# Optimization experiments

Hardware: AMD Instinct MI355X
Metric: run time of the kernel (lower is better)

Reference implementation:

```python
import jax, jax.numpy as jnp
import numpy as np

S, B, DM, H, DFF = 2048, 4, 1024, 16, 4096
DK = DM // H  # 64, dv == dk
EPS = 1e-5

def layer_norm(x, g, b):
    mu = jnp.mean(x, axis=-1, keepdims=True)
    var = jnp.var(x, axis=-1, keepdims=True)
    return (x - mu) * jax.lax.rsqrt(var + EPS) * g + b

def setup_inputs() -> dict:
    key = jax.random.key(0)
    ks = jax.random.split(key, 12)
    sc = 0.02
    return {
        "X": jax.random.normal(ks[0], (S, B, DM), dtype=jnp.float32),
        # stacked per-head projections: weight [H, dk, dm], bias [H, dk]
        "WQ_w": jax.random.normal(ks[1], (H, DK, DM), dtype=jnp.float32) * sc,
        "WQ_b": jnp.zeros((H, DK), dtype=jnp.float32),
        "WK_w": jax.random.normal(ks[2], (H, DK, DM), dtype=jnp.float32) * sc,
        "WK_b": jnp.zeros((H, DK), dtype=jnp.float32),
        "WV_w": jax.random.normal(ks[3], (H, DK, DM), dtype=jnp.float32) * sc,
        "WV_b": jnp.zeros((H, DK), dtype=jnp.float32),
        "WO_w": jax.random.normal(ks[4], (DM, H * DK), dtype=jnp.float32) * sc,
        "WO_b": jnp.zeros((DM,), dtype=jnp.float32),
        "ln1_g": jnp.ones((DM,), dtype=jnp.float32),
        "ln1_b": jnp.zeros((DM,), dtype=jnp.float32),
        "W1": jax.random.normal(ks[5], (DFF, DM), dtype=jnp.float32) * sc,
        "b1": jnp.zeros((DFF,), dtype=jnp.float32),
        "W2": jax.random.normal(ks[6], (DM, DFF), dtype=jnp.float32) * sc,
        "b2": jnp.zeros((DM,), dtype=jnp.float32),
        "ln2_g": jnp.ones((DM,), dtype=jnp.float32),
        "ln2_b": jnp.zeros((DM,), dtype=jnp.float32),
    }

def reference(X, WQ_w, WQ_b, WK_w, WK_b, WV_w, WV_b, WO_w, WO_b,
              ln1_g, ln1_b, W1, b1, W2, b2, ln2_g, ln2_b):
    # --- self-attention (encoder: no causal mask, no key_mask, drop=0) ---
    # X: [S, B, DM]; per-head Q/K/V: [S, B, H, DK]
    Q = jnp.einsum('sbd,hkd->sbhk', X, WQ_w) + WQ_b
    K = jnp.einsum('sbd,hkd->sbhk', X, WK_w) + WK_b
    V = jnp.einsum('sbd,hvd->sbhv', X, WV_w) + WV_b
    scores = jnp.einsum('sbhk,lbhk->sbhl', Q, K) / jnp.sqrt(jnp.float32(DK))
    attn = jax.nn.softmax(scores, axis=-1)  # softmax over keys l
    ctx = jnp.einsum('sbhl,lbhv->sbhv', attn, V)
    # concat heads (head-major order matches torch.concat over head list)
    ctx = ctx.reshape(S, B, H * DK)
    y = ctx @ WO_w.T + WO_b
    X1 = layer_norm(y + X, ln1_g, ln1_b)
    # --- MLP (1 hidden layer, ReLU) ---
    h = jax.nn.relu(X1 @ W1.T + b1)
    m = h @ W2.T + b2
    return layer_norm(m + X1, ln2_g, ln2_b)
```

## Files before the change

kernel.cpp:

```cpp
#include <hip/hip_runtime.h>
#include <stdint.h>

typedef short bf16x8 __attribute__((ext_vector_type(8)));
typedef float f32x4 __attribute__((ext_vector_type(4)));
typedef float f32x16 __attribute__((ext_vector_type(16)));

__device__ __forceinline__ float bf2f(uint16_t u) {
    union { uint32_t i; float f; } c; c.i = ((uint32_t)u) << 16; return c.f;
}
__device__ __forceinline__ uint16_t f2bf(float f) {
    union { float f; uint32_t i; } c; c.f = f;
    uint32_t x = c.i;
    return (uint16_t)((x + 0x7fffu + ((x >> 16) & 1u)) >> 16);
}
__device__ __forceinline__ uint32_t pack2t(float lo, float hi) {
    union { float f; uint32_t u; } a, b;
    a.f = lo; b.f = hi;
    return __builtin_amdgcn_perm(b.u, a.u, 0x07060302u);
}

__device__ __forceinline__ float exp2r(float x) {
#if __has_builtin(__builtin_amdgcn_exp2f)
    return __builtin_amdgcn_exp2f(x);
#else
    return exp2f(x);
#endif
}

__device__ __forceinline__ void plane32_swap(uint32_t& a, uint32_t& b) {
#if __has_builtin(__builtin_amdgcn_permlane32_swap)
    typedef unsigned int u32x2 __attribute__((ext_vector_type(2)));
    u32x2 r = __builtin_amdgcn_permlane32_swap(a, b, false, false);
    a = r[0]; b = r[1];
#else
    asm volatile("v_permlane32_swap_b32 %0, %1" : "+v"(a), "+v"(b));
#endif
}

__device__ __forceinline__ void load_lds16(const void* g, void* lds) {
    using gp_t = const __attribute__((address_space(1))) uint32_t*;
    using lp_t = __attribute__((address_space(3))) uint32_t*;
    __builtin_amdgcn_global_load_lds(
        reinterpret_cast<gp_t>(reinterpret_cast<uintptr_t>(g)),
        reinterpret_cast<lp_t>((uint32_t)reinterpret_cast<uintptr_t>(lds)),
        16, 0, 0);
}

__global__ __launch_bounds__(256) void cvt_all(
    const float* __restrict__ X,
    const float* __restrict__ wqf, const float* __restrict__ wkf,
    const float* __restrict__ wvf, const float* __restrict__ wof,
    const float* __restrict__ w1f, const float* __restrict__ w2f,
    const float* __restrict__ bqf, const float* __restrict__ bkf,
    const float* __restrict__ bvf, const float* __restrict__ bof,
    const float* __restrict__ b1f, const float* __restrict__ b2f,
    uint16_t* __restrict__ Xb, uint16_t* __restrict__ wd, uint16_t* __restrict__ bd)
{
    const int b = blockIdx.x, tid = threadIdx.x;
    const size_t M = 1048576ull;
    const float* s; uint16_t* d; size_t i, off;
    if (b < 8192) {
        i = ((size_t)b * 256 + tid) * 4;
        s = X; off = i; d = Xb;
    } else if (b < 20480) {
        i = ((size_t)(b - 8192) * 256 + tid) * 4;
        d = wd;
        if (i < M)           { s = wqf; off = i; }
        else if (i < 2 * M)  { s = wkf; off = i - M; }
        else if (i < 3 * M)  { s = wvf; off = i - 2 * M; }
        else if (i < 4 * M)  { s = wof; off = i - 3 * M; }
        else if (i < 8 * M)  { s = w1f; off = i - 4 * M; }
        else                 { s = w2f; off = i - 8 * M; }
    } else {
        int j = tid * 4;
        d = bd;
        for (int p = 0; p < 9; ++p, j += 1024) {
            const float* sb; int ob;
            if (j < 1024)      { sb = bqf; ob = j; }
            else if (j < 2048) { sb = bkf; ob = j - 1024; }
            else if (j < 3072) { sb = bvf; ob = j - 2048; }
            else if (j < 4096) { sb = bof; ob = j - 3072; }
            else if (j < 8192) { sb = b1f; ob = j - 4096; }
            else               { sb = b2f; ob = j - 8192; }
            float4 x = *(const float4*)(sb + ob);
            ushort4 u;
            u.x = f2bf(x.x); u.y = f2bf(x.y); u.z = f2bf(x.z); u.w = f2bf(x.w);
            *(ushort4*)(d + j) = u;
        }
        return;
    }
    float4 x = *(const float4*)(s + off);
    ushort4 u;
    u.x = f2bf(x.x); u.y = f2bf(x.y); u.z = f2bf(x.z); u.w = f2bf(x.w);
    *(ushort4*)(d + i) = u;
}

template<int MODE, int NT>
__global__ __launch_bounds__(256) void gemm_bt(
    const uint16_t* __restrict__ A, const uint16_t* __restrict__ B,
    const uint16_t* __restrict__ bias, uint16_t* __restrict__ C,
    int K, int N, int relu)
{
    const int CT = NT / 32;
    __shared__ uint16_t sA[128 * 64];
    __shared__ uint16_t sB[NT * 64];
    const int tid = threadIdx.x;
    const int w = tid >> 6, ln = tid & 63;
    const int m = ln & 15, q = ln >> 4;
    const int wr = w >> 1, wc = w & 1;
    const int tm = blockIdx.y * 128, tn = blockIdx.x * NT;

    f32x4 zero = {0.f, 0.f, 0.f, 0.f};
    f32x4 acc[4][CT];
#pragma unroll
    for (int i = 0; i < 4; ++i)
#pragma unroll
        for (int j = 0; j < CT; ++j) acc[i][j] = zero;

    const int sr = tid >> 3;
    const int sc_ = tid & 7;
    const int g = sc_ ^ (sr & 7);

    for (int k0 = 0; k0 < K; k0 += 64) {
        __syncthreads();
#pragma unroll
        for (int i = 0; i < 4; ++i) {
            int r = i * 32 + sr;
            load_lds16(A + (size_t)(tm + r) * K + k0 + g * 8, &sA[(i * 32 + w * 8) * 64]);
        }
#pragma unroll
        for (int i = 0; i < NT / 32; ++i) {
            int r = i * 32 + sr;
            load_lds16(B + (size_t)(tn + r) * K + k0 + g * 8, &sB[(i * 32 + w * 8) * 64]);
        }
        __syncthreads();
#pragma unroll
        for (int kk = 0; kk < 2; ++kk) {
            bf16x8 af[4], bfr[CT];
            const int s = (kk * 4 + q) ^ (m & 7);
#pragma unroll
            for (int rt = 0; rt < 4; ++rt) {
                int R = wr * 64 + rt * 16 + m;
                af[rt] = *(const bf16x8*)&sA[R * 64 + s * 8];
            }
#pragma unroll
            for (int ct = 0; ct < CT; ++ct) {
                int R = wc * (NT / 2) + ct * 16 + m;
                bfr[ct] = *(const bf16x8*)&sB[R * 64 + s * 8];
            }
#pragma unroll
            for (int rt = 0; rt < 4; ++rt)
#pragma unroll
                for (int ct = 0; ct < CT; ++ct)
                    acc[rt][ct] = __builtin_amdgcn_mfma_f32_16x16x32_bf16(
                        af[rt], bfr[ct], acc[rt][ct], 0, 0, 0);
        }
    }

#pragma unroll
    for (int ct = 0; ct < CT; ++ct) {
        int col = tn + wc * (NT / 2) + ct * 16 + m;
        float bv = bf2f(bias[col]);
#pragma unroll
        for (int rt = 0; rt < 4; ++rt) {
            int rowb = tm + wr * 64 + rt * 16 + q * 4;
#pragma unroll
            for (int rg = 0; rg < 4; ++rg) {
                int t = rowb + rg;
                float v = acc[rt][ct][rg] + bv;
                if (relu) v = fmaxf(v, 0.f);
                C[(size_t)t * N + col] = f2bf(v);
            }
        }
    }
}

template<int MODE>
__global__ __launch_bounds__(512, 2) void gemm8(
    const uint16_t* __restrict__ A, const uint16_t* __restrict__ B,
    const uint16_t* __restrict__ bias, uint16_t* __restrict__ C,
    int K, int N, int NBX, int relu)
{
    extern __shared__ uint16_t smem[];

    const int tid = threadIdx.x;
    const int w = tid >> 6, ln = tid & 63;
    const int m = ln & 15, q = ln >> 4;
    const int wr = w >> 2, wc = w & 3;

    const int nwg = gridDim.x;
    const int bid = blockIdx.x;
    const int wg = (bid & 7) * (nwg >> 3) + (bid >> 3);
    const int bx = wg % NBX, by = wg / NBX;
    const int tm = by * 256, tn = bx * 256;

    const int sr = tid >> 3;
    const int g = (tid & 7) ^ (sr & 7);
    const int wbase = w * 512;

    const int KT = K >> 6;

    f32x4 acc[8][4];
#pragma unroll
    for (int i = 0; i < 8; ++i)
#pragma unroll
        for (int j = 0; j < 4; ++j) acc[i][j] = f32x4{0.f, 0.f, 0.f, 0.f};

    auto stage2 = [&](int buf, int t, int i0) {
        uint16_t* dA = smem + buf * 16384;
        uint16_t* dB = smem + 32768 + buf * 16384;
#pragma unroll
        for (int i = i0; i < i0 + 2; ++i) {
            load_lds16(A + (size_t)(tm + i * 64 + sr) * K + t * 64 + g * 8,
                       dA + i * 4096 + wbase);
            load_lds16(B + (size_t)(tn + i * 64 + sr) * K + t * 64 + g * 8,
                       dB + i * 4096 + wbase);
        }
    };

    stage2(0, 0, 0);
    stage2(0, 0, 2);
    asm volatile("s_waitcnt vmcnt(0)" ::: "memory");
    __builtin_amdgcn_s_barrier();

    for (int t = 0; t < KT; ++t) {
        const int cur = t & 1;
        const uint16_t* pA = smem + cur * 16384;
        const uint16_t* pB = smem + 32768 + cur * 16384;
        const bool pf = (t + 1 < KT);

        bf16x8 bfrag[4], afrag[4];

        {
            const int s = q ^ (m & 7);
#pragma unroll
            for (int nf = 0; nf < 4; ++nf)
                bfrag[nf] = *(const bf16x8*)&pB[(wc * 64 + nf * 16 + m) * 64 + s * 8];
#pragma unroll
            for (int mf = 0; mf < 4; ++mf)
                afrag[mf] = *(const bf16x8*)&pA[(wr * 128 + mf * 16 + m) * 64 + s * 8];
        }
        if (pf) stage2(cur ^ 1, t + 1, 0);
        __builtin_amdgcn_s_barrier();
        asm volatile("s_waitcnt lgkmcnt(0)" ::: "memory");
        __builtin_amdgcn_sched_barrier(0);
        __builtin_amdgcn_s_setprio(1);
#pragma unroll
        for (int mf = 0; mf < 4; ++mf)
#pragma unroll
            for (int nf = 0; nf < 4; ++nf)
                acc[mf][nf] = __builtin_amdgcn_mfma_f32_16x16x32_bf16(
                    afrag[mf], bfrag[nf], acc[mf][nf], 0, 0, 0);
        __builtin_amdgcn_s_setprio(0);
        __builtin_amdgcn_s_barrier();

        {
            const int s = q ^ (m & 7);
#pragma unroll
            for (int mf = 0; mf < 4; ++mf)
                afrag[mf] = *(const bf16x8*)&pA[(wr * 128 + (mf + 4) * 16 + m) * 64 + s * 8];
        }
        if (pf) stage2(cur ^ 1, t + 1, 2);
        __builtin_amdgcn_s_barrier();
        asm volatile("s_waitcnt lgkmcnt(0)" ::: "memory");
        __builtin_amdgcn_sched_barrier(0);
        __builtin_amdgcn_s_setprio(1);
#pragma unroll
        for (int mf = 0; mf < 4; ++mf)
#pragma unroll
            for (int nf = 0; nf < 4; ++nf)
                acc[mf + 4][nf] = __builtin_amdgcn_mfma_f32_16x16x32_bf16(
                    afrag[mf], bfrag[nf], acc[mf + 4][nf], 0, 0, 0);
        __builtin_amdgcn_s_setprio(0);
        __builtin_amdgcn_s_barrier();

        {
            const int s = (4 + q) ^ (m & 7);
#pragma unroll
            for (int nf = 0; nf < 4; ++nf)
                bfrag[nf] = *(const bf16x8*)&pB[(wc * 64 + nf * 16 + m) * 64 + s * 8];
#pragma unroll
            for (int mf = 0; mf < 4; ++mf)
                afrag[mf] = *(const bf16x8*)&pA[(wr * 128 + mf * 16 + m) * 64 + s * 8];
        }
        __builtin_amdgcn_s_barrier();
        asm volatile("s_waitcnt lgkmcnt(0)" ::: "memory");
        __builtin_amdgcn_sched_barrier(0);
        __builtin_amdgcn_s_setprio(1);
#pragma unroll
        for (int mf = 0; mf < 4; ++mf)
#pragma unroll
            for (int nf = 0; nf < 4; ++nf)
                acc[mf][nf] = __builtin_amdgcn_mfma_f32_16x16x32_bf16(
                    afrag[mf], bfrag[nf], acc[mf][nf], 0, 0, 0);
        __builtin_amdgcn_s_setprio(0);
        __builtin_amdgcn_s_barrier();

        {
            const int s = (4 + q) ^ (m & 7);
#pragma unroll
            for (int mf = 0; mf < 4; ++mf)
                afrag[mf] = *(const bf16x8*)&pA[(wr * 128 + (mf + 4) * 16 + m) * 64 + s * 8];
        }
        __builtin_amdgcn_s_barrier();
        asm volatile("s_waitcnt lgkmcnt(0)" ::: "memory");
        __builtin_amdgcn_sched_barrier(0);
        __builtin_amdgcn_s_setprio(1);
#pragma unroll
        for (int mf = 0; mf < 4; ++mf)
#pragma unroll
            for (int nf = 0; nf < 4; ++nf)
                acc[mf + 4][nf] = __builtin_amdgcn_mfma_f32_16x16x32_bf16(
                    afrag[mf], bfrag[nf], acc[mf + 4][nf], 0, 0, 0);
        __builtin_amdgcn_s_setprio(0);
        if (pf) asm volatile("s_waitcnt vmcnt(0)" ::: "memory");
        __builtin_amdgcn_s_barrier();
    }

    const int sect = tn >> 10;
#pragma unroll
    for (int nf = 0; nf < 4; ++nf) {
        int col = tn + wc * 64 + nf * 16 + m;
        float bv = bf2f(bias[col]);
#pragma unroll
        for (int mf = 0; mf < 8; ++mf) {
            int rowb = tm + wr * 128 + mf * 16 + q * 4;
#pragma unroll
            for (int rg = 0; rg < 4; ++rg) {
                int t = rowb + rg;
                float v = acc[mf][nf][rg] + bv;
                if (relu) v = fmaxf(v, 0.f);
                size_t off;
                if (MODE == 0) {
                    off = (size_t)t * N + col;
                } else {
                    int c = col & 1023;
                    int bh = (t & 3) * 16 + (c >> 6);
                    if (sect == 0) {
                        off = (size_t)bh * 131072 + (t >> 2) * 64 + (c & 63);
                        v *= 0.18033688f;
                    } else if (sect == 1) {
                        off = 8388608ull + (size_t)bh * 131072 + (t >> 2) * 64 + (c & 63);
                    } else {
                        off = 16777216ull + (size_t)bh * 131072 + (size_t)(c & 63) * 2048 + (t >> 2);
                    }
                }
                C[off] = f2bf(v);
            }
        }
    }
}

__global__ __launch_bounds__(256) void attn2(
    const uint16_t* __restrict__ Qh, const uint16_t* __restrict__ Kh,
    const uint16_t* __restrict__ Vt, uint16_t* __restrict__ CTX)
{
    __shared__ uint16_t sK[2][64 * 64];
    __shared__ uint16_t sV[2][64 * 64];

    const int tid = threadIdx.x;
    const int w = tid >> 6, ln = tid & 63;
    const int m5 = ln & 31, h5 = ln >> 5;
    const int bh = blockIdx.x, qt = blockIdx.y;
    const uint16_t* Qb = Qh + (size_t)bh * 131072;
    const uint16_t* Kb = Kh + (size_t)bh * 131072;
    const uint16_t* Vb = Vt + (size_t)bh * 131072;

    const int qrow = qt * 128 + w * 32 + m5;
    bf16x8 qf[4];
#pragma unroll
    for (int ks = 0; ks < 4; ++ks)
        qf[ks] = *(const bf16x8*)(Qb + (size_t)qrow * 64 + ks * 16 + h5 * 8);

    f32x16 Oa[2];
#pragma unroll
    for (int nb = 0; nb < 2; ++nb)
#pragma unroll
        for (int i = 0; i < 16; ++i) Oa[nb][i] = 0.f;
    float psum = 0.f;

    const int sr = tid >> 3;
    const int g = (tid & 7) ^ (sr & 7);

    {
        load_lds16(Kb + (size_t)sr * 64 + g * 8,            &sK[0][tid * 8]);
        load_lds16(Kb + (size_t)(sr + 32) * 64 + g * 8,     &sK[0][2048 + tid * 8]);
        load_lds16(Vb + (size_t)sr * 2048 + g * 8,          &sV[0][tid * 8]);
        load_lds16(Vb + (size_t)(sr + 32) * 2048 + g * 8,   &sV[0][2048 + tid * 8]);
    }

    for (int c = 0; c < 32; ++c) {
        const int cur = c & 1;
        __syncthreads();
        if (c + 1 < 32) {
            const int nc = c + 1;
            uint16_t* kd = &sK[cur ^ 1][0];
            uint16_t* vd = &sV[cur ^ 1][0];
            load_lds16(Kb + (size_t)(nc * 64 + sr) * 64 + g * 8,        kd + tid * 8);
            load_lds16(Kb + (size_t)(nc * 64 + sr + 32) * 64 + g * 8,   kd + 2048 + tid * 8);
            load_lds16(Vb + (size_t)sr * 2048 + nc * 64 + g * 8,        vd + tid * 8);
            load_lds16(Vb + (size_t)(sr + 32) * 2048 + nc * 64 + g * 8, vd + 2048 + tid * 8);
        }

        bf16x8 pf[4];
#pragma unroll
        for (int kb = 0; kb < 2; ++kb) {
            f32x16 acc;
#pragma unroll
            for (int i = 0; i < 16; ++i) acc[i] = 0.f;
#pragma unroll
            for (int ks = 0; ks < 4; ++ks) {
                int row = kb * 32 + m5;
                int ph = (2 * ks + h5) ^ (m5 & 7);
                bf16x8 kf = *(const bf16x8*)&sK[cur][row * 64 + ph * 8];
                acc = __builtin_amdgcn_mfma_f32_32x32x16_bf16(kf, qf[ks], acc, 0, 0, 0);
            }
#pragma unroll
            for (int ksl = 0; ksl < 2; ++ksl) {
                float p0 = exp2r(acc[8 * ksl + 0]);
                float p1 = exp2r(acc[8 * ksl + 1]);
                float p2 = exp2r(acc[8 * ksl + 2]);
                float p3 = exp2r(acc[8 * ksl + 3]);
                float p4 = exp2r(acc[8 * ksl + 4]);
                float p5 = exp2r(acc[8 * ksl + 5]);
                float p6 = exp2r(acc[8 * ksl + 6]);
                float p7 = exp2r(acc[8 * ksl + 7]);
                psum += ((p0 + p1) + (p2 + p3)) + ((p4 + p5) + (p6 + p7));
                uint32_t x0 = pack2t(p0, p1);
                uint32_t x1 = pack2t(p2, p3);
                uint32_t y0 = pack2t(p4, p5);
                uint32_t y1 = pack2t(p6, p7);
                plane32_swap(x0, y0);
                plane32_swap(x1, y1);
                union { uint32_t u[4]; bf16x8 v; } pu;
                pu.u[0] = x0; pu.u[1] = x1; pu.u[2] = y0; pu.u[3] = y1;
                pf[kb * 2 + ksl] = pu.v;
            }
        }

#pragma unroll
        for (int ks = 0; ks < 4; ++ks) {
#pragma unroll
            for (int nb = 0; nb < 2; ++nb) {
                int vrow = nb * 32 + m5;
                int ph = (2 * ks + h5) ^ (m5 & 7);
                bf16x8 vf = *(const bf16x8*)&sV[cur][vrow * 64 + ph * 8];
                Oa[nb] = __builtin_amdgcn_mfma_f32_32x32x16_bf16(pf[ks], vf, Oa[nb], 0, 0, 0);
            }
        }
    }

    float l = psum + __shfl_xor(psum, 32);
    float linv = 1.f / l;
    float li[16];
#pragma unroll
    for (int a = 0; a < 4; ++a)
#pragma unroll
        for (int r = 0; r < 4; ++r)
            li[4 * a + r] = __shfl(linv, r + 8 * a + 4 * h5);

    const int b_ = bh >> 4, h_ = bh & 15;
#pragma unroll
    for (int nb = 0; nb < 2; ++nb)
#pragma unroll
        for (int a = 0; a < 4; ++a)
#pragma unroll
            for (int r = 0; r < 4; ++r) {
                int qr = r + 8 * a + 4 * h5;
                int s = qt * 128 + w * 32 + qr;
                int col = h_ * 64 + nb * 32 + m5;
                CTX[(size_t)(s * 4 + b_) * 1024 + col] = f2bf(Oa[nb][4 * a + r] * li[4 * a + r]);
            }
}

template<bool RES_F32, bool OUT_F32>
__global__ __launch_bounds__(256) void ln_resid(
    const uint16_t* __restrict__ Y, const void* __restrict__ Xp,
    const float* __restrict__ G, const float* __restrict__ Bv,
    void* __restrict__ Op)
{
    const int row = blockIdx.x, tid = threadIdx.x;
    const size_t base = (size_t)row * 1024 + tid * 4;
    ushort4 yv = *(const ushort4*)(Y + base);
    float x0, x1, x2, x3;
    if (RES_F32) {
        float4 xv = *(const float4*)((const float*)Xp + base);
        x0 = xv.x; x1 = xv.y; x2 = xv.z; x3 = xv.w;
    } else {
        ushort4 xv = *(const ushort4*)((const uint16_t*)Xp + base);
        x0 = bf2f(xv.x); x1 = bf2f(xv.y); x2 = bf2f(xv.z); x3 = bf2f(xv.w);
    }
    float v0 = bf2f(yv.x) + x0;
    float v1 = bf2f(yv.y) + x1;
    float v2 = bf2f(yv.z) + x2;
    float v3 = bf2f(yv.w) + x3;
    float s = v0 + v1 + v2 + v3;
    float ss = v0 * v0 + v1 * v1 + v2 * v2 + v3 * v3;
#pragma unroll
    for (int off = 32; off > 0; off >>= 1) {
        s += __shfl_down(s, off);
        ss += __shfl_down(ss, off);
    }
    __shared__ float rs[4], rss[4];
    if ((tid & 63) == 0) { rs[tid >> 6] = s; rss[tid >> 6] = ss; }
    __syncthreads();
    float S = rs[0] + rs[1] + rs[2] + rs[3];
    float SS = rss[0] + rss[1] + rss[2] + rss[3];
    const float invn = 1.f / 1024.f;
    float mu = S * invn;
    float var = SS * invn - mu * mu;
    float rstd = rsqrtf(var + 1e-5f);
    float4 gv = *(const float4*)(G + tid * 4);
    float4 bv = *(const float4*)(Bv + tid * 4);
    float o0 = (v0 - mu) * rstd * gv.x + bv.x;
    float o1 = (v1 - mu) * rstd * gv.y + bv.y;
    float o2 = (v2 - mu) * rstd * gv.z + bv.z;
    float o3 = (v3 - mu) * rstd * gv.w + bv.w;
    if (OUT_F32) {
        float4 o = {o0, o1, o2, o3};
        *(float4*)((float*)Op + base) = o;
    } else {
        ushort4 o;
        o.x = f2bf(o0); o.y = f2bf(o1); o.z = f2bf(o2); o.w = f2bf(o3);
        *(ushort4*)((uint16_t*)Op + base) = o;
    }
}

extern "C" void kernel_launch(void* const* d_in, const int* in_sizes, int n_in,
                              void* d_out, int out_size, void* d_ws, size_t ws_size,
                              hipStream_t stream)
{
    const float* X    = (const float*)d_in[0];
    const float* WQw  = (const float*)d_in[1];
    const float* WQb  = (const float*)d_in[2];
    const float* WKw  = (const float*)d_in[3];
    const float* WKb  = (const float*)d_in[4];
    const float* WVw  = (const float*)d_in[5];
    const float* WVb  = (const float*)d_in[6];
    const float* WOw  = (const float*)d_in[7];
    const float* WOb  = (const float*)d_in[8];
    const float* ln1g = (const float*)d_in[9];
    const float* ln1b = (const float*)d_in[10];
    const float* W1   = (const float*)d_in[11];
    const float* b1   = (const float*)d_in[12];
    const float* W2   = (const float*)d_in[13];
    const float* b2   = (const float*)d_in[14];
    const float* ln2g = (const float*)d_in[15];
    const float* ln2b = (const float*)d_in[16];

    uint16_t* ws = (uint16_t*)d_ws;
    const size_t E = 8192ull * 1024ull;
    const size_t MW = 1048576ull;
    uint16_t* Xb   = ws;
    uint16_t* qh   = ws + E;
    uint16_t* kh   = ws + 2 * E;
    uint16_t* vt   = ws + 3 * E;
    uint16_t* ctx  = ws + 4 * E;
    uint16_t* y    = qh;
    uint16_t* x1   = kh;
    uint16_t* m2   = vt;
    uint16_t* hbuf = ws + 5 * E;
    uint16_t* wq   = ws + 9 * E;
    uint16_t* wo   = wq + 3 * MW;
    uint16_t* w1   = wo + MW;
    uint16_t* w2   = w1 + 4 * MW;
    uint16_t* bq   = w2 + 4 * MW;
    uint16_t* bo   = bq + 3072;
    uint16_t* bb1  = bo + 1024;
    uint16_t* bb2  = bb1 + 4096;

    static bool attr_set = false;
    if (!attr_set) {
        (void)hipFuncSetAttribute(reinterpret_cast<const void*>(gemm8<3>),
                                  hipFuncAttributeMaxDynamicSharedMemorySize, 131072);
        (void)hipFuncSetAttribute(reinterpret_cast<const void*>(gemm8<0>),
                                  hipFuncAttributeMaxDynamicSharedMemorySize, 131072);
        attr_set = true;
    }

    cvt_all<<<dim3(20481), dim3(256), 0, stream>>>(
        X, WQw, WKw, WVw, WOw, W1, W2, WQb, WKb, WVb, WOb, b1, b2,
        Xb, wq, bq);

    dim3 blk(256);
    gemm8<3><<<dim3(384), dim3(512), 131072, stream>>>(Xb, wq, bq, qh, 1024, 3072, 12, 0);
    attn2<<<dim3(64, 16), blk, 0, stream>>>(qh, kh, vt, ctx);
    gemm_bt<0, 64><<<dim3(16, 64),  blk, 0, stream>>>(ctx,  wo, bo,  y,    1024, 1024, 0);
    ln_resid<true, false><<<dim3(8192), blk, 0, stream>>>(y, X, ln1g, ln1b, x1);
    gemm8<0><<<dim3(512), dim3(512), 131072, stream>>>(x1, w1, bb1, hbuf, 1024, 4096, 16, 1);
    gemm_bt<0, 64><<<dim3(16, 64),  blk, 0, stream>>>(hbuf, w2, bb2, m2,   4096, 1024, 0);
    ln_resid<false, true><<<dim3(8192), blk, 0, stream>>>(m2, x1, ln2g, ln2b, d_out);
}
```

Before: 557.0 us.

## Shrink gemm8 tile to 256x128 with triple-buffered LDS prefetch two steps ahead

The bf16 MFMA GEMM tile shrinks from 256x256 to 256x128. Eight waves are now arranged 4x2, and each wave holds a 4x4 accumulator array instead of 8x4. The LDS pipeline moves from double buffering to a three-buffer ring that prefetches K-tile t+2 while computing t, using partial vmcnt waits so loads overlap more. Grid sizes double for the QKV and W1 GEMMs. This should raise occupancy and latency hiding, at the cost of more LDS per block (144 KB, which allows only one block per CU) and less data reuse per tile.

```diff
diff --git a/kernel.cpp b/kernel.cpp
--- a/kernel.cpp
+++ b/kernel.cpp
@@ -186,61 +186,62 @@
     const int tid = threadIdx.x;
     const int w = tid >> 6, ln = tid & 63;
     const int m = ln & 15, q = ln >> 4;
-    const int wr = w >> 2, wc = w & 3;
+    const int wr = w >> 1, wc = w & 1;
 
     const int nwg = gridDim.x;
     const int bid = blockIdx.x;
     const int wg = (bid & 7) * (nwg >> 3) + (bid >> 3);
     const int bx = wg % NBX, by = wg / NBX;
-    const int tm = by * 256, tn = bx * 256;
+    const int tm = by * 256, tn = bx * 128;
 
     const int sr = tid >> 3;
     const int g = (tid & 7) ^ (sr & 7);
     const int wbase = w * 512;
-
     const int KT = K >> 6;
 
-    f32x4 acc[8][4];
-#pragma unroll
-    for (int i = 0; i < 8; ++i)
+    f32x4 acc[4][4];
+#pragma unroll
+    for (int i = 0; i < 4; ++i)
 #pragma unroll
         for (int j = 0; j < 4; ++j) acc[i][j] = f32x4{0.f, 0.f, 0.f, 0.f};
 
-    auto stage2 = [&](int buf, int t, int i0) {
-        uint16_t* dA = smem + buf * 16384;
-        uint16_t* dB = smem + 32768 + buf * 16384;
-#pragma unroll
-        for (int i = i0; i < i0 + 2; ++i) {
+    auto stageA2 = [&](int buf, int t, int i0) {
+        uint16_t* dA = smem + buf * 24576;
+#pragma unroll
+        for (int i = i0; i < i0 + 2; ++i)
             load_lds16(A + (size_t)(tm + i * 64 + sr) * K + t * 64 + g * 8,
                        dA + i * 4096 + wbase);
-            load_lds16(B + (size_t)(tn + i * 64 + sr) * K + t * 64 + g * 8,
-                       dB + i * 4096 + wbase);
-        }
     };
-
-    stage2(0, 0, 0);
-    stage2(0, 0, 2);
-    asm volatile("s_waitcnt vmcnt(0)" ::: "memory");
+    auto stageB1 = [&](int buf, int t, int i) {
+        uint16_t* dB = smem + buf * 24576 + 16384;
+        load_lds16(B + (size_t)(tn + i * 64 + sr) * K + t * 64 + g * 8,
+                   dB + i * 4096 + wbase);
+    };
+
+    stageA2(0, 0, 0); stageA2(0, 0, 2); stageB1(0, 0, 0); stageB1(0, 0, 1);
+    stageA2(1, 1, 0); stageA2(1, 1, 2); stageB1(1, 1, 0); stageB1(1, 1, 1);
+    asm volatile("s_waitcnt vmcnt(6)" ::: "memory");
     __builtin_amdgcn_s_barrier();
 
+    int bufc = 0;
     for (int t = 0; t < KT; ++t) {
-        const int cur = t & 1;
-        const uint16_t* pA = smem + cur * 16384;
-        const uint16_t* pB = smem + 32768 + cur * 16384;
-        const bool pf = (t + 1 < KT);
-
-        bf16x8 bfrag[4], afrag[4];
+        const uint16_t* pA = smem + bufc * 24576;
+        const uint16_t* pB = pA + 16384;
+        int bufn = bufc + 2; if (bufn >= 3) bufn -= 3;
+        const bool pf = (t + 2 < KT);
+
+        bf16x8 af[4], bfr[4];
 
         {
             const int s = q ^ (m & 7);
 #pragma unroll
+            for (int mf = 0; mf < 4; ++mf)
+                af[mf] = *(const bf16x8*)&pA[(wr * 64 + mf * 16 + m) * 64 + s * 8];
+#pragma unroll
             for (int nf = 0; nf < 4; ++nf)
-                bfrag[nf] = *(const bf16x8*)&pB[(wc * 64 + nf * 16 + m) * 64 + s * 8];
-#pragma unroll
-            for (int mf = 0; mf < 4; ++mf)
-                afrag[mf] = *(const bf16x8*)&pA[(wr * 128 + mf * 16 + m) * 64 + s * 8];
-        }
-        if (pf) stage2(cur ^ 1, t + 1, 0);
+                bfr[nf] = *(const bf16x8*)&pB[(wc * 64 + nf * 16 + m) * 64 + s * 8];
+        }
+        if (pf) { stageA2(bufn, t + 2, 0); stageB1(bufn, t + 2, 0); }
         __builtin_amdgcn_s_barrier();
         asm volatile("s_waitcnt lgkmcnt(0)" ::: "memory");
         __builtin_amdgcn_sched_barrier(0);
@@ -250,17 +251,20 @@
 #pragma unroll
             for (int nf = 0; nf < 4; ++nf)
                 acc[mf][nf] = __builtin_amdgcn_mfma_f32_16x16x32_bf16(
-                    afrag[mf], bfrag[nf], acc[mf][nf], 0, 0, 0);
+                    af[mf], bfr[nf], acc[mf][nf], 0, 0, 0);
         __builtin_amdgcn_s_setprio(0);
         __builtin_amdgcn_s_barrier();
 
         {
-            const int s = q ^ (m & 7);
+            const int s = (4 + q) ^ (m & 7);
 #pragma unroll
             for (int mf = 0; mf < 4; ++mf)
-                afrag[mf] = *(const bf16x8*)&pA[(wr * 128 + (mf + 4) * 16 + m) * 64 + s * 8];
-        }
-        if (pf) stage2(cur ^ 1, t + 1, 2);
+                af[mf] = *(const bf16x8*)&pA[(wr * 64 + mf * 16 + m) * 64 + s * 8];
+#pragma unroll
+            for (int nf = 0; nf < 4; ++nf)
+                bfr[nf] = *(const bf16x8*)&pB[(wc * 64 + nf * 16 + m) * 64 + s * 8];
+        }
+        if (pf) { stageA2(bufn, t + 2, 2); stageB1(bufn, t + 2, 1); }
         __builtin_amdgcn_s_barrier();
         asm volatile("s_waitcnt lgkmcnt(0)" ::: "memory");
         __builtin_amdgcn_sched_barrier(0);
@@ -269,52 +273,15 @@
         for (int mf = 0; mf < 4; ++mf)
 #pragma unroll
             for (int nf = 0; nf < 4; ++nf)
-                acc[mf + 4][nf] = __builtin_amdgcn_mfma_f32_16x16x32_bf16(
-                    afrag[mf], bfrag[nf], acc[mf + 4][nf], 0, 0, 0);
+                acc[mf][nf] = __builtin_amdgcn_mfma_f32_16x16x32_bf16(
+                    af[mf], bfr[nf], acc[mf][nf], 0, 0, 0);
         __builtin_amdgcn_s_setprio(0);
+        if (t + 1 < KT) {
+            if (pf) asm volatile("s_waitcnt vmcnt(6)" ::: "memory");
+            else    asm volatile("s_waitcnt vmcnt(0)" ::: "memory");
+        }
         __builtin_amdgcn_s_barrier();
-
-        {
-            const int s = (4 + q) ^ (m & 7);
-#pragma unroll
-            for (int nf = 0; nf < 4; ++nf)
-                bfrag[nf] = *(const bf16x8*)&pB[(wc * 64 + nf * 16 + m) * 64 + s * 8];
-#pragma unroll
-            for (int mf = 0; mf < 4; ++mf)
-                afrag[mf] = *(const bf16x8*)&pA[(wr * 128 + mf * 16 + m) * 64 + s * 8];
-        }
-        __builtin_amdgcn_s_barrier();
-        asm volatile("s_waitcnt lgkmcnt(0)" ::: "memory");
-        __builtin_amdgcn_sched_barrier(0);
-        __builtin_amdgcn_s_setprio(1);
-#pragma unroll
-        for (int mf = 0; mf < 4; ++mf)
-#pragma unroll
-            for (int nf = 0; nf < 4; ++nf)
-                acc[mf][nf] = __builtin_amdgcn_mfma_f32_16x16x32_bf16(
-                    afrag[mf], bfrag[nf], acc[mf][nf], 0, 0, 0);
-        __builtin_amdgcn_s_setprio(0);
-        __builtin_amdgcn_s_barrier();
-
-        {
-            const int s = (4 + q) ^ (m & 7);
-#pragma unroll
-            for (int mf = 0; mf < 4; ++mf)
-                afrag[mf] = *(const bf16x8*)&pA[(wr * 128 + (mf + 4) * 16 + m) * 64 + s * 8];
-        }
-        __builtin_amdgcn_s_barrier();
-        asm volatile("s_waitcnt lgkmcnt(0)" ::: "memory");
-        __builtin_amdgcn_sched_barrier(0);
-        __builtin_amdgcn_s_setprio(1);
-#pragma unroll
-        for (int mf = 0; mf < 4; ++mf)
-#pragma unroll
-            for (int nf = 0; nf < 4; ++nf)
-                acc[mf + 4][nf] = __builtin_amdgcn_mfma_f32_16x16x32_bf16(
-                    afrag[mf], bfrag[nf], acc[mf + 4][nf], 0, 0, 0);
-        __builtin_amdgcn_s_setprio(0);
-        if (pf) asm volatile("s_waitcnt vmcnt(0)" ::: "memory");
-        __builtin_amdgcn_s_barrier();
+        bufc = (bufc + 1 == 3) ? 0 : bufc + 1;
     }
 
     const int sect = tn >> 10;
@@ -323,8 +290,8 @@
         int col = tn + wc * 64 + nf * 16 + m;
         float bv = bf2f(bias[col]);
 #pragma unroll
-        for (int mf = 0; mf < 8; ++mf) {
-            int rowb = tm + wr * 128 + mf * 16 + q * 4;
+        for (int mf = 0; mf < 4; ++mf) {
+            int rowb = tm + wr * 64 + mf * 16 + q * 4;
 #pragma unroll
             for (int rg = 0; rg < 4; ++rg) {
                 int t = rowb + rg;
@@ -572,9 +539,9 @@
     static bool attr_set = false;
     if (!attr_set) {
         (void)hipFuncSetAttribute(reinterpret_cast<const void*>(gemm8<3>),
-                                  hipFuncAttributeMaxDynamicSharedMemorySize, 131072);
+                                  hipFuncAttributeMaxDynamicSharedMemorySize, 147456);
         (void)hipFuncSetAttribute(reinterpret_cast<const void*>(gemm8<0>),
-                                  hipFuncAttributeMaxDynamicSharedMemorySize, 131072);
+                                  hipFuncAttributeMaxDynamicSharedMemorySize, 147456);
         attr_set = true;
     }
 
@@ -583,11 +550,11 @@
         Xb, wq, bq);
 
     dim3 blk(256);
-    gemm8<3><<<dim3(384), dim3(512), 131072, stream>>>(Xb, wq, bq, qh, 1024, 3072, 12, 0);
+    gemm8<3><<<dim3(768), dim3(512), 147456, stream>>>(Xb, wq, bq, qh, 1024, 3072, 24, 0);
     attn2<<<dim3(64, 16), blk, 0, stream>>>(qh, kh, vt, ctx);
     gemm_bt<0, 64><<<dim3(16, 64),  blk, 0, stream>>>(ctx,  wo, bo,  y,    1024, 1024, 0);
     ln_resid<true, false><<<dim3(8192), blk, 0, stream>>>(y, X, ln1g, ln1b, x1);
-    gemm8<0><<<dim3(512), dim3(512), 131072, stream>>>(x1, w1, bb1, hbuf, 1024, 4096, 16, 1);
+    gemm8<0><<<dim3(1024), dim3(512), 147456, stream>>>(x1, w1, bb1, hbuf, 1024, 4096, 32, 1);
     gemm_bt<0, 64><<<dim3(16, 64),  blk, 0, stream>>>(hbuf, w2, bb2, m2,   4096, 1024, 0);
     ln_resid<false, true><<<dim3(8192), blk, 0, stream>>>(m2, x1, ln2g, ln2b, d_out);
 }
```

Result: faster. 534.4 us (-4.1%).
